# Kernel optimization log

Measured on AMD Instinct MI355X. Metric: run time of the kernel, lower is better.

The kernel has to match this reference:

```python
import jax, jax.numpy as jnp
import numpy as np
import math

D_HEAD = 64
D_MODEL = 1024
N_HEADS = D_MODEL // D_HEAD
MAX_TOKENS = 2048
BATCH = 4
SEQ = 2048


def setup_inputs() -> dict:
    key = jax.random.key(0)
    k1, k2, k3, k4, k5 = jax.random.split(key, 5)
    residual_stream = jax.random.normal(k1, (BATCH, SEQ, D_MODEL), dtype=jnp.float32)
    # kaiming_normal_ (fan_in = d_model for [head, d_model, d_head] with default mode)
    std_qkv = math.sqrt(2.0 / D_MODEL)
    weight_query = jax.random.normal(k2, (N_HEADS, D_MODEL, D_HEAD), dtype=jnp.float32) * std_qkv
    weight_key = jax.random.normal(k3, (N_HEADS, D_MODEL, D_HEAD), dtype=jnp.float32) * std_qkv
    weight_value = jax.random.normal(k4, (N_HEADS, D_MODEL, D_HEAD), dtype=jnp.float32) * std_qkv
    # xavier_normal_ for [d_model, d_model]
    std_out = math.sqrt(2.0 / (D_MODEL + D_MODEL))
    weight_out = jax.random.normal(k5, (D_MODEL, D_MODEL), dtype=jnp.float32) * std_out
    return {
        "residual_stream": residual_stream,
        "weight_query": weight_query,
        "weight_key": weight_key,
        "weight_value": weight_value,
        "weight_out": weight_out,
    }


def reference(residual_stream, weight_query, weight_key, weight_value, weight_out):
    # residual_stream: [b, s, m]; weights: [h, m, d]
    q = jnp.einsum("bsm,hmd->bhsd", residual_stream, weight_query)
    k = jnp.einsum("bsm,hmd->bhsd", residual_stream, weight_key)
    v = jnp.einsum("bsm,hmd->bhsd", residual_stream, weight_value)
    scores = jnp.einsum("bhqd,bhkd->bhqk", q, k) / math.sqrt(D_HEAD)  # [b,h,s,s]
    n = scores.shape[-1]
    causal = jnp.tril(jnp.ones((n, n), dtype=bool))
    scores = jnp.where(causal, scores, -jnp.inf)
    attn = jax.nn.softmax(scores, axis=-1)
    out = jnp.einsum("bhqk,bhkd->bhqd", attn, v)  # [b,h,s,d]
    b, h, s, d = out.shape
    concat = out.transpose(0, 2, 1, 3).reshape(b, s, h * d)  # [b,s,m]
    return jnp.einsum("bsm,mn->bsn", concat, weight_out)
```

## Files before the change

kernel.cpp:

```cpp
#include <hip/hip_runtime.h>
#include <hip/hip_bf16.h>
#include <math.h>

#define BATCH 4
#define SEQ   2048
#define DM    1024
#define NH    16
#define DH    64

#define QSCALE 0.1803368801111204f

typedef __bf16 bf16x8 __attribute__((ext_vector_type(8)));
typedef __bf16 bf16x4 __attribute__((ext_vector_type(4)));
typedef float  f32x4  __attribute__((ext_vector_type(4)));

typedef const __attribute__((address_space(1))) unsigned int guint;
typedef __attribute__((address_space(3)))       unsigned int luint;

__device__ __forceinline__ void async16(const __bf16* g, __bf16* l) {
    __builtin_amdgcn_global_load_lds((guint*)g, (luint*)l, 16, 0, 0);
}

__device__ __forceinline__ float fast_exp2(float x) {
#if __has_builtin(__builtin_amdgcn_exp2f)
    return __builtin_amdgcn_exp2f(x);
#else
    float r; asm("v_exp_f32 %0, %1" : "=v"(r) : "v"(x)); return r;
#endif
}
__device__ __forceinline__ float fast_rcp(float x) {
#if __has_builtin(__builtin_amdgcn_rcpf)
    return __builtin_amdgcn_rcpf(x);
#else
    float r; asm("v_rcp_f32 %0, %1" : "=v"(r) : "v"(x)); return r;
#endif
}

__device__ __forceinline__ bf16x8 load8f(const float* __restrict__ base, size_t idx) {
    const float4 a = *(const float4*)(base + idx);
    const float4 b = *(const float4*)(base + idx + 4);
    bf16x8 r;
    r[0] = (__bf16)a.x; r[1] = (__bf16)a.y; r[2] = (__bf16)a.z; r[3] = (__bf16)a.w;
    r[4] = (__bf16)b.x; r[5] = (__bf16)b.y; r[6] = (__bf16)b.z; r[7] = (__bf16)b.w;
    return r;
}

__global__ __launch_bounds__(256)
void prep_kernel(const float* __restrict__ X,
                 const float* __restrict__ Wq,
                 const float* __restrict__ Wk,
                 const float* __restrict__ Wv,
                 const float* __restrict__ Wo,
                 __bf16* __restrict__ Xb,
                 __bf16* __restrict__ Wqt,
                 __bf16* __restrict__ Wkt,
                 __bf16* __restrict__ Wvt,
                 __bf16* __restrict__ Wot)
{
    __shared__ __bf16 T[64][65];
    const int t  = threadIdx.x;
    const int bx = blockIdx.x;

    if (bx < 4096) {
        size_t idx = ((size_t)bx * 256 + t) * 8;
        *(bf16x8*)&Xb[idx] = load8f(X, idx);
        return;
    }

    const float* src;
    __bf16* dst;
    int k0, n0, srcN;
    if (bx < 4096 + 768) {
        const int i = bx - 4096;
        const int z = i >> 4;
        const int m = z >> 4;
        const int h = z & 15;
        src  = (m == 0 ? Wq : m == 1 ? Wk : Wv) + (size_t)h * DM * DH;
        dst  = (m == 0 ? Wqt : m == 1 ? Wkt : Wvt) + (size_t)h * DH * DM;
        k0   = (i & 15) * 64;
        n0   = 0;
        srcN = DH;
    } else {
        const int i = bx - 4096 - 768;
        src  = Wo;
        dst  = Wot;
        k0   = (i & 15) * 64;
        n0   = (i >> 4) * 64;
        srcN = DM;
    }

#pragma unroll
    for (int i = 0; i < 4; ++i) {
        int row = i * 16 + (t >> 4);
        int col = (t & 15) * 4;
        float4 v = *(const float4*)&src[(size_t)(k0 + row) * srcN + n0 + col];
        T[col + 0][row] = (__bf16)v.x;
        T[col + 1][row] = (__bf16)v.y;
        T[col + 2][row] = (__bf16)v.z;
        T[col + 3][row] = (__bf16)v.w;
    }
    __syncthreads();
#pragma unroll
    for (int i = 0; i < 4; ++i) {
        int n  = i * 16 + (t >> 4);
        int kc = (t & 15) * 4;
        bf16x4 v;
        v[0] = T[n][kc + 0]; v[1] = T[n][kc + 1];
        v[2] = T[n][kc + 2]; v[3] = T[n][kc + 3];
        *(bf16x4*)&dst[(size_t)(n0 + n) * DM + k0 + kc] = v;
    }
}

__global__ __launch_bounds__(256)
void qkv_gemm(const __bf16* __restrict__ Xb,
              const __bf16* __restrict__ Wcat,
              __bf16* __restrict__ Qo,
              __bf16* __restrict__ Ko,
              __bf16* __restrict__ Vto)
{
    const int rowTile = blockIdx.x;
    const int colTile = blockIdx.y;
    const int r0 = rowTile * 128;
    const int n0 = colTile * 128;

    __shared__ __align__(16) __bf16 As[128 * 32];
    __shared__ __align__(16) __bf16 Bs[128 * 32];

    const int t    = threadIdx.x;
    const int wave = t >> 6;
    const int lane = t & 63;
    const int l15  = lane & 15;
    const int quad = lane >> 4;

    f32x4 acc[2][8];
#pragma unroll
    for (int s = 0; s < 2; ++s)
#pragma unroll
        for (int i = 0; i < 8; ++i) acc[s][i] = (f32x4){0.f, 0.f, 0.f, 0.f};

    const int lrow = lane >> 2;
    const int lcol = (lane & 3) * 8;

    for (int k0 = 0; k0 < DM; k0 += 32) {
        __syncthreads();
#pragma unroll
        for (int c = 0; c < 2; ++c) {
            const int rb = wave * 32 + c * 16;
            async16(&Xb  [(size_t)(r0 + rb + lrow) * DM + k0 + lcol], &As[rb * 32]);
            async16(&Wcat[(size_t)(n0 + rb + lrow) * DM + k0 + lcol], &Bs[rb * 32]);
        }
        __syncthreads();

        bf16x8 a0 = *(const bf16x8*)&As[(wave * 16 + l15) * 32 + quad * 8];
        bf16x8 a1 = *(const bf16x8*)&As[(64 + wave * 16 + l15) * 32 + quad * 8];
#pragma unroll
        for (int ct = 0; ct < 8; ++ct) {
            bf16x8 bb = *(const bf16x8*)&Bs[(ct * 16 + l15) * 32 + quad * 8];
            acc[0][ct] = __builtin_amdgcn_mfma_f32_16x16x32_bf16(a0, bb, acc[0][ct], 0, 0, 0);
            acc[1][ct] = __builtin_amdgcn_mfma_f32_16x16x32_bf16(a1, bb, acc[1][ct], 0, 0, 0);
        }
    }

    const int mat = colTile >> 3;
    if (mat < 2) {
        __bf16* __restrict__ Dst = (mat == 0) ? Qo : Ko;
        const float scale = (mat == 0) ? QSCALE : 1.0f;
#pragma unroll
        for (int st = 0; st < 2; ++st) {
            const int r = r0 + st * 64 + wave * 16 + quad * 4;
            const int b = r >> 11;
            const int s = r & (SEQ - 1);
#pragma unroll
            for (int ct = 0; ct < 8; ++ct) {
                const int n = (n0 + ct * 16 + l15) & 1023;
                const int h = n >> 6;
                const int d = n & 63;
                const size_t base = (((size_t)(b * NH + h)) * SEQ + s) * DH + d;
#pragma unroll
                for (int reg = 0; reg < 4; ++reg)
                    Dst[base + (size_t)reg * DH] = (__bf16)(acc[st][ct][reg] * scale);
            }
        }
    } else {
#pragma unroll
        for (int st = 0; st < 2; ++st) {
            const int r = r0 + st * 64 + wave * 16 + quad * 4;
            const int b = r >> 11;
            const int s = r & (SEQ - 1);
#pragma unroll
            for (int ct = 0; ct < 8; ++ct) {
                const int n = (n0 + ct * 16 + l15) & 1023;
                const int h = n >> 6;
                const int d = n & 63;
                bf16x4 vv;
                vv[0] = (__bf16)acc[st][ct][0]; vv[1] = (__bf16)acc[st][ct][1];
                vv[2] = (__bf16)acc[st][ct][2]; vv[3] = (__bf16)acc[st][ct][3];
                *(bf16x4*)&Vto[(((size_t)(b * NH + h)) * DH + d) * SEQ + s] = vv;
            }
        }
    }
}

__global__ __launch_bounds__(256)
void attn_kernel(const __bf16* __restrict__ Q,
                 const __bf16* __restrict__ K,
                 const __bf16* __restrict__ Vt,
                 __bf16* __restrict__ Cat)
{
    const int x   = blockIdx.x;
    const int qtA = x;
    const int qtB = 31 - x;
    const int bh  = blockIdx.y;
    const int b   = bh >> 4;
    const int h   = bh & 15;

    const __bf16* Qg  = Q  + (size_t)bh * SEQ * DH;
    const __bf16* Kg  = K  + (size_t)bh * SEQ * DH;
    const __bf16* Vtg = Vt + (size_t)bh * DH * SEQ;

    __shared__ __align__(16) __bf16 Ks[64 * 72];
    __shared__ __align__(16) __bf16 Vs[64 * 72];
    __shared__ __align__(16) __bf16 Ps[64 * 72];

    const int t    = threadIdx.x;
    const int wave = t >> 6;
    const int lane = t & 63;
    const int l15  = lane & 15;
    const int quad = lane >> 4;

    bf16x8 qfA[2], qfB[2];
    {
        const size_t rA = (size_t)(qtA * 64 + wave * 16 + l15);
        qfA[0] = *(const bf16x8*)&Qg[rA * DH + quad * 8];
        qfA[1] = *(const bf16x8*)&Qg[rA * DH + 32 + quad * 8];
        const size_t rB = (size_t)(qtB * 64 + wave * 16 + l15);
        qfB[0] = *(const bf16x8*)&Qg[rB * DH + quad * 8];
        qfB[1] = *(const bf16x8*)&Qg[rB * DH + 32 + quad * 8];
    }

    bf16x8 ones;
#pragma unroll
    for (int j = 0; j < 8; ++j) ones[j] = (__bf16)1.0f;

    f32x4 oA[4], oB[4], olA, olB;
#pragma unroll
    for (int ct = 0; ct < 4; ++ct) {
        oA[ct] = (f32x4){0.f, 0.f, 0.f, 0.f};
        oB[ct] = (f32x4){0.f, 0.f, 0.f, 0.f};
    }
    olA = (f32x4){0.f, 0.f, 0.f, 0.f};
    olB = (f32x4){0.f, 0.f, 0.f, 0.f};

    const int srow0 = t >> 3;
    const int scol  = (t & 7) * 8;
    bf16x8 kreg[2], vreg[2];
#pragma unroll
    for (int i = 0; i < 2; ++i) {
        int row = srow0 + i * 32;
        kreg[i] = *(const bf16x8*)&Kg[(size_t)row * DH + scol];
        vreg[i] = *(const bf16x8*)&Vtg[(size_t)row * SEQ + scol];
    }

    auto half_step = [&](const bf16x8* qf, f32x4* o, f32x4& ol, bool diag) {
        f32x4 sc[4];
        __builtin_amdgcn_s_setprio(1);
#pragma unroll
        for (int ct = 0; ct < 4; ++ct) {
            sc[ct] = (f32x4){0.f, 0.f, 0.f, 0.f};
            bf16x8 b0 = *(const bf16x8*)&Ks[(ct * 16 + l15) * 72 + quad * 8];
            sc[ct] = __builtin_amdgcn_mfma_f32_16x16x32_bf16(qf[0], b0, sc[ct], 0, 0, 0);
            bf16x8 b1 = *(const bf16x8*)&Ks[(ct * 16 + l15) * 72 + 32 + quad * 8];
            sc[ct] = __builtin_amdgcn_mfma_f32_16x16x32_bf16(qf[1], b1, sc[ct], 0, 0, 0);
        }
        __builtin_amdgcn_s_setprio(0);
        if (diag) {
#pragma unroll
            for (int ct = 0; ct < 4; ++ct)
#pragma unroll
                for (int r = 0; r < 4; ++r) {
                    int qr = wave * 16 + quad * 4 + r;
                    int kc = ct * 16 + l15;
                    if (kc > qr) sc[ct][r] = -INFINITY;
                }
        }
#pragma unroll
        for (int ct = 0; ct < 4; ++ct)
#pragma unroll
            for (int r = 0; r < 4; ++r)
                sc[ct][r] = fast_exp2(sc[ct][r]);

#pragma unroll
        for (int ct = 0; ct < 4; ++ct)
#pragma unroll
            for (int r = 0; r < 4; ++r)
                Ps[(wave * 16 + quad * 4 + r) * 72 + ct * 16 + l15] =
                    (__bf16)sc[ct][r];

        bf16x8 af0 = *(const bf16x8*)&Ps[(wave * 16 + l15) * 72 + quad * 8];
        bf16x8 af1 = *(const bf16x8*)&Ps[(wave * 16 + l15) * 72 + 32 + quad * 8];

        __builtin_amdgcn_s_setprio(1);
#pragma unroll
        for (int ct = 0; ct < 4; ++ct) {
            bf16x8 v0 = *(const bf16x8*)&Vs[(ct * 16 + l15) * 72 + quad * 8];
            o[ct] = __builtin_amdgcn_mfma_f32_16x16x32_bf16(af0, v0, o[ct], 0, 0, 0);
            bf16x8 v1 = *(const bf16x8*)&Vs[(ct * 16 + l15) * 72 + 32 + quad * 8];
            o[ct] = __builtin_amdgcn_mfma_f32_16x16x32_bf16(af1, v1, o[ct], 0, 0, 0);
        }
        ol = __builtin_amdgcn_mfma_f32_16x16x32_bf16(af0, ones, ol, 0, 0, 0);
        ol = __builtin_amdgcn_mfma_f32_16x16x32_bf16(af1, ones, ol, 0, 0, 0);
        __builtin_amdgcn_s_setprio(0);
    };

    for (int kt = 0; kt <= qtB; ++kt) {
        __syncthreads();
#pragma unroll
        for (int i = 0; i < 2; ++i) {
            int row = srow0 + i * 32;
            *(bf16x8*)&Ks[row * 72 + scol] = kreg[i];
            *(bf16x8*)&Vs[row * 72 + scol] = vreg[i];
        }
        __syncthreads();

        {
            const int kvn = (kt < qtB ? kt + 1 : kt) * 64;
#pragma unroll
            for (int i = 0; i < 2; ++i) {
                int row = srow0 + i * 32;
                kreg[i] = *(const bf16x8*)&Kg[(size_t)(kvn + row) * DH + scol];
                vreg[i] = *(const bf16x8*)&Vtg[(size_t)row * SEQ + kvn + scol];
            }
        }

        half_step(qfB, oB, olB, kt == qtB);
        if (kt <= qtA)
            half_step(qfA, oA, olA, kt == qtA);
    }

#pragma unroll
    for (int ct = 0; ct < 4; ++ct)
#pragma unroll
        for (int r = 0; r < 4; ++r) {
            int rr = wave * 16 + quad * 4 + r;
            int sA = qtA * 64 + rr;
            int sB = qtB * 64 + rr;
            Cat[((size_t)(b * SEQ + sA)) * DM + h * DH + ct * 16 + l15] =
                (__bf16)(oA[ct][r] * fast_rcp(olA[r]));
            Cat[((size_t)(b * SEQ + sB)) * DM + h * DH + ct * 16 + l15] =
                (__bf16)(oB[ct][r] * fast_rcp(olB[r]));
        }
}

__global__ __launch_bounds__(256)
void oproj_kernel(const __bf16* __restrict__ A,
                  const __bf16* __restrict__ Wot,
                  float* __restrict__ C)
{
    const int rowTile = blockIdx.x;
    const int colTile = blockIdx.y;
    const int r0 = rowTile * 128;
    const int n0 = colTile * 128;

    __shared__ __align__(16) __bf16 As[128 * 32];
    __shared__ __align__(16) __bf16 Bs[128 * 32];

    const int t    = threadIdx.x;
    const int wave = t >> 6;
    const int lane = t & 63;
    const int l15  = lane & 15;
    const int quad = lane >> 4;

    f32x4 acc[2][8];
#pragma unroll
    for (int s = 0; s < 2; ++s)
#pragma unroll
        for (int i = 0; i < 8; ++i) acc[s][i] = (f32x4){0.f, 0.f, 0.f, 0.f};

    const int lrow = lane >> 2;
    const int lcol = (lane & 3) * 8;

    for (int k0 = 0; k0 < DM; k0 += 32) {
        __syncthreads();
#pragma unroll
        for (int c = 0; c < 2; ++c) {
            const int rb = wave * 32 + c * 16;
            async16(&A  [(size_t)(r0 + rb + lrow) * DM + k0 + lcol], &As[rb * 32]);
            async16(&Wot[(size_t)(n0 + rb + lrow) * DM + k0 + lcol], &Bs[rb * 32]);
        }
        __syncthreads();

        bf16x8 a0 = *(const bf16x8*)&As[(wave * 16 + l15) * 32 + quad * 8];
        bf16x8 a1 = *(const bf16x8*)&As[(64 + wave * 16 + l15) * 32 + quad * 8];
#pragma unroll
        for (int ct = 0; ct < 8; ++ct) {
            bf16x8 bb = *(const bf16x8*)&Bs[(ct * 16 + l15) * 32 + quad * 8];
            acc[0][ct] = __builtin_amdgcn_mfma_f32_16x16x32_bf16(a0, bb, acc[0][ct], 0, 0, 0);
            acc[1][ct] = __builtin_amdgcn_mfma_f32_16x16x32_bf16(a1, bb, acc[1][ct], 0, 0, 0);
        }
    }

#pragma unroll
    for (int st = 0; st < 2; ++st)
#pragma unroll
        for (int ct = 0; ct < 8; ++ct)
#pragma unroll
            for (int reg = 0; reg < 4; ++reg) {
                int r = r0 + st * 64 + wave * 16 + quad * 4 + reg;
                int n = n0 + ct * 16 + l15;
                C[(size_t)r * DM + n] = acc[st][ct][reg];
            }
}

extern "C" void kernel_launch(void* const* d_in, const int* in_sizes, int n_in,
                              void* d_out, int out_size, void* d_ws, size_t ws_size,
                              hipStream_t stream)
{
    (void)in_sizes; (void)n_in; (void)out_size; (void)ws_size;
    const float* X  = (const float*)d_in[0];
    const float* Wq = (const float*)d_in[1];
    const float* Wk = (const float*)d_in[2];
    const float* Wv = (const float*)d_in[3];
    const float* Wo = (const float*)d_in[4];
    float* out = (float*)d_out;

    char* ws = (char*)d_ws;
    const size_t wqkv_b = (size_t)NH * DM * DH * sizeof(__bf16);
    const size_t wo_b   = (size_t)DM * DM * sizeof(__bf16);
    const size_t big_b  = (size_t)BATCH * NH * SEQ * DH * sizeof(__bf16);
    __bf16* Wqt = (__bf16*)(ws);
    __bf16* Wkt = (__bf16*)(ws + wqkv_b);
    __bf16* Wvt = (__bf16*)(ws + 2 * wqkv_b);
    __bf16* Wot = (__bf16*)(ws + 3 * wqkv_b);
    __bf16* Qb  = (__bf16*)(ws + 3 * wqkv_b + wo_b);
    __bf16* Kb  = (__bf16*)(ws + 3 * wqkv_b + wo_b + big_b);
    __bf16* Vtb = (__bf16*)(ws + 3 * wqkv_b + wo_b + 2 * big_b);
    __bf16* Cat = (__bf16*)(ws + 3 * wqkv_b + wo_b + 3 * big_b);
    __bf16* Xb  = (__bf16*)(ws + 3 * wqkv_b + wo_b + 4 * big_b);

    prep_kernel<<<dim3(4096 + 768 + 256), 256, 0, stream>>>(
        X, Wq, Wk, Wv, Wo, Xb, Wqt, Wkt, Wvt, Wot);
    qkv_gemm<<<dim3(64, 24), 256, 0, stream>>>(Xb, Wqt, Qb, Kb, Vtb);
    attn_kernel<<<dim3(16, 64), 256, 0, stream>>>(Qb, Kb, Vtb, Cat);
    oproj_kernel<<<dim3(64, 8), 256, 0, stream>>>(Cat, Wot, out);
}
```

Measured before the change: 263.5 us.

## Stage Q/K epilogue through swizzled LDS and read V fragments directly from global

The QKV GEMM epilogue for Q and K now writes accumulators into a per-wave XOR-swizzled LDS slab, then emits 16-byte vector stores instead of scattered scalar bf16 stores. In the attention kernel, V is no longer staged through shared memory: each half-step loads its V^T fragments straight from global (or L2) into registers. It also adds a min-blocks hint of 4 on the attention kernel. This removes uncoalesced scalar stores and an LDS buffer plus its writes, at the cost of redundant global V reads (once per half-step) and possible register pressure under the tighter launch bound.

```diff
diff --git a/kernel.cpp b/kernel.cpp
--- a/kernel.cpp
+++ b/kernel.cpp
@@ -123,8 +123,9 @@
     const int r0 = rowTile * 128;
     const int n0 = colTile * 128;
 
-    __shared__ __align__(16) __bf16 As[128 * 32];
-    __shared__ __align__(16) __bf16 Bs[128 * 32];
+    __shared__ __align__(16) __bf16 SM[8192];
+    __bf16* As = SM;
+    __bf16* Bs = SM + 4096;
 
     const int t    = threadIdx.x;
     const int wave = t >> 6;
@@ -165,20 +166,32 @@
     if (mat < 2) {
         __bf16* __restrict__ Dst = (mat == 0) ? Qo : Ko;
         const float scale = (mat == 0) ? QSCALE : 1.0f;
+        __syncthreads();
+        char* slab = (char*)SM + wave * 4096;
+        const int nb = n0 & 1023;
 #pragma unroll
         for (int st = 0; st < 2; ++st) {
-            const int r = r0 + st * 64 + wave * 16 + quad * 4;
-            const int b = r >> 11;
-            const int s = r & (SEQ - 1);
-#pragma unroll
-            for (int ct = 0; ct < 8; ++ct) {
-                const int n = (n0 + ct * 16 + l15) & 1023;
-                const int h = n >> 6;
-                const int d = n & 63;
-                const size_t base = (((size_t)(b * NH + h)) * SEQ + s) * DH + d;
-#pragma unroll
-                for (int reg = 0; reg < 4; ++reg)
-                    Dst[base + (size_t)reg * DH] = (__bf16)(acc[st][ct][reg] * scale);
+#pragma unroll
+            for (int ct = 0; ct < 8; ++ct)
+#pragma unroll
+                for (int reg = 0; reg < 4; ++reg) {
+                    const int row = quad * 4 + reg;
+                    *(__bf16*)(slab + row * 256 +
+                               (((ct * 16 + l15) * 2) ^ ((row & 7) << 4))) =
+                        (__bf16)(acc[st][ct][reg] * scale);
+                }
+#pragma unroll
+            for (int i = 0; i < 4; ++i) {
+                const int row = i * 4 + quad;
+                bf16x8 w = *(const bf16x8*)(slab + row * 256 +
+                                            ((l15 * 16) ^ ((row & 7) << 4)));
+                const int rg = r0 + st * 64 + wave * 16 + row;
+                const int b  = rg >> 11;
+                const int s  = rg & (SEQ - 1);
+                const int nn = nb + l15 * 8;
+                const int h  = nn >> 6;
+                const int d  = nn & 63;
+                *(bf16x8*)&Dst[(((size_t)(b * NH + h)) * SEQ + s) * DH + d] = w;
             }
         }
     } else {
@@ -201,7 +214,7 @@
     }
 }
 
-__global__ __launch_bounds__(256)
+__global__ __launch_bounds__(256, 4)
 void attn_kernel(const __bf16* __restrict__ Q,
                  const __bf16* __restrict__ K,
                  const __bf16* __restrict__ Vt,
@@ -219,7 +232,6 @@
     const __bf16* Vtg = Vt + (size_t)bh * DH * SEQ;
 
     __shared__ __align__(16) __bf16 Ks[64 * 72];
-    __shared__ __align__(16) __bf16 Vs[64 * 72];
     __shared__ __align__(16) __bf16 Ps[64 * 72];
 
     const int t    = threadIdx.x;
@@ -253,15 +265,22 @@
 
     const int srow0 = t >> 3;
     const int scol  = (t & 7) * 8;
-    bf16x8 kreg[2], vreg[2];
+    bf16x8 kreg[2];
 #pragma unroll
     for (int i = 0; i < 2; ++i) {
         int row = srow0 + i * 32;
         kreg[i] = *(const bf16x8*)&Kg[(size_t)row * DH + scol];
-        vreg[i] = *(const bf16x8*)&Vtg[(size_t)row * SEQ + scol];
-    }
-
-    auto half_step = [&](const bf16x8* qf, f32x4* o, f32x4& ol, bool diag) {
+    }
+
+    auto half_step = [&](const bf16x8* qf, f32x4* o, f32x4& ol, bool diag, int k0v) {
+        bf16x8 vf0[4], vf1[4];
+#pragma unroll
+        for (int ct = 0; ct < 4; ++ct) {
+            const size_t vrow = (size_t)(ct * 16 + l15) * SEQ + k0v;
+            vf0[ct] = *(const bf16x8*)&Vtg[vrow + quad * 8];
+            vf1[ct] = *(const bf16x8*)&Vtg[vrow + 32 + quad * 8];
+        }
+
         f32x4 sc[4];
         __builtin_amdgcn_s_setprio(1);
 #pragma unroll
@@ -302,10 +321,8 @@
         __builtin_amdgcn_s_setprio(1);
 #pragma unroll
         for (int ct = 0; ct < 4; ++ct) {
-            bf16x8 v0 = *(const bf16x8*)&Vs[(ct * 16 + l15) * 72 + quad * 8];
-            o[ct] = __builtin_amdgcn_mfma_f32_16x16x32_bf16(af0, v0, o[ct], 0, 0, 0);
-            bf16x8 v1 = *(const bf16x8*)&Vs[(ct * 16 + l15) * 72 + 32 + quad * 8];
-            o[ct] = __builtin_amdgcn_mfma_f32_16x16x32_bf16(af1, v1, o[ct], 0, 0, 0);
+            o[ct] = __builtin_amdgcn_mfma_f32_16x16x32_bf16(af0, vf0[ct], o[ct], 0, 0, 0);
+            o[ct] = __builtin_amdgcn_mfma_f32_16x16x32_bf16(af1, vf1[ct], o[ct], 0, 0, 0);
         }
         ol = __builtin_amdgcn_mfma_f32_16x16x32_bf16(af0, ones, ol, 0, 0, 0);
         ol = __builtin_amdgcn_mfma_f32_16x16x32_bf16(af1, ones, ol, 0, 0, 0);
@@ -318,7 +335,6 @@
         for (int i = 0; i < 2; ++i) {
             int row = srow0 + i * 32;
             *(bf16x8*)&Ks[row * 72 + scol] = kreg[i];
-            *(bf16x8*)&Vs[row * 72 + scol] = vreg[i];
         }
         __syncthreads();
 
@@ -328,13 +344,12 @@
             for (int i = 0; i < 2; ++i) {
                 int row = srow0 + i * 32;
                 kreg[i] = *(const bf16x8*)&Kg[(size_t)(kvn + row) * DH + scol];
-                vreg[i] = *(const bf16x8*)&Vtg[(size_t)row * SEQ + kvn + scol];
             }
         }
 
-        half_step(qfB, oB, olB, kt == qtB);
+        half_step(qfB, oB, olB, kt == qtB, kt * 64);
         if (kt <= qtA)
-            half_step(qfA, oA, olA, kt == qtA);
+            half_step(qfA, oA, olA, kt == qtA, kt * 64);
     }
 
 #pragma unroll
```

After: 385.7 us. +46.4%, slower.
